# Performance work log

Measured on AMD Instinct MI355X. Metric: run time of the kernel, lower is better.

Reference implementation:

```python
import jax, jax.numpy as jnp
import numpy as np

C = 1.0          # self.c = -curvature = 1.0
SQRT_C = 1.0
EPS = 1e-10
NORM_MAX = 0.99


def setup_inputs() -> dict:
    key = jax.random.key(0)
    k1, k2 = jax.random.split(key)
    b, n, m, d = 4, 4096, 4096, 128
    # scale so points lie inside the Poincare ball (||x|| ~ 0.57 < 1)
    x = jax.random.normal(k1, (b, n, d), dtype=jnp.float32) * 0.05
    y = jax.random.normal(k2, (b, m, d), dtype=jnp.float32) * 0.05
    return {"x": x, "y": y}


def reference(x, y):
    # Pairwise hyperbolic distance d(x_i, y_j) = 2/sqrt(c) * atanh(sqrt(c) * ||(-x_i) (+)_c y_j||)
    # Mobius add: num = A*(-x) + B*y, denom = 1 + 2c<-x,y> + c^2 ||x||^2 ||y||^2
    # with A = 1 + 2c<-x,y> + c||y||^2,  B = 1 - c||x||^2.
    # We never form the (b,n,m,d) tensor: ||A*(-x)+B*y||^2 = A^2||x||^2 - 2AB<x,y> + B^2||y||^2.
    xs = jnp.sum(x * x, axis=-1)                     # (b, n)
    ys = jnp.sum(y * y, axis=-1)                     # (b, m)
    dot = jnp.einsum('bnd,bmd->bnm', x, y)           # (b, n, m) <x_i, y_j>
    xs_ = xs[:, :, None]                             # (b, n, 1)
    ys_ = ys[:, None, :]                             # (b, 1, m)
    A = 1.0 - 2.0 * C * dot + C * ys_                # (b, n, m)
    B = 1.0 - C * xs_                                # (b, n, 1)
    denom = 1.0 - 2.0 * C * dot + (C * C) * xs_ * ys_
    num_sq = A * A * xs_ - 2.0 * A * B * dot + B * B * ys_
    diff_norm = jnp.sqrt(jnp.maximum(num_sq, 0.0)) / jnp.maximum(denom, EPS)
    diff_norm = jnp.clip(diff_norm, EPS, NORM_MAX)
    return (2.0 / SQRT_C) * jnp.arctanh(SQRT_C * diff_norm)
```

## Files before the change

kernel.cpp:

```cpp
#include <hip/hip_runtime.h>
#include <hip/hip_bf16.h>

typedef __bf16 bf16x8 __attribute__((ext_vector_type(8)));
typedef float  f32x4  __attribute__((ext_vector_type(4)));

#define NN 4096
#define DK 128
#define BM 128
#define BN 128
#define NMAX 0.99f
#define LN2F 0.69314718056f

#define WS_XB   0
#define WS_YB   (4u*4096u*DK*2u)
#define WS_XC   (2u*WS_YB)
#define WS_YC   (WS_XC + 4u*4096u*8u)
#define WS_REQ  (WS_YC + 4u*4096u*8u)

__device__ __forceinline__ void load_lds16(const void* g, void* l) {
    __builtin_amdgcn_global_load_lds(
        (const __attribute__((address_space(1))) unsigned int*)g,
        (__attribute__((address_space(3))) unsigned int*)l, 16, 0, 0);
}

__global__ __launch_bounds__(256)
void prep_kernel(const float* __restrict__ X, const float* __restrict__ Y,
                 __bf16* __restrict__ Xb, __bf16* __restrict__ Yb,
                 float2* __restrict__ XC, float2* __restrict__ YC)
{
    const int tid = threadIdx.x;
    const int c16 = tid & 15;
    const int rl  = tid >> 4;
    const int gr  = blockIdx.x * 16 + rl;

    const float* src = blockIdx.y ? Y : X;
    __bf16*      dst = blockIdx.y ? Yb : Xb;
    float2*      nc  = blockIdx.y ? YC : XC;

    const f32x4* s4 = (const f32x4*)(src + (size_t)gr * DK + c16 * 8);
    f32x4 v0 = s4[0], v1 = s4[1];
    float s = v0[0]*v0[0] + v0[1]*v0[1] + v0[2]*v0[2] + v0[3]*v0[3]
            + v1[0]*v1[0] + v1[1]*v1[1] + v1[2]*v1[2] + v1[3]*v1[3];
    s += __shfl_xor(s, 1);
    s += __shfl_xor(s, 2);
    s += __shfl_xor(s, 4);
    s += __shfl_xor(s, 8);

    bf16x8 pk;
    pk[0]=(__bf16)v0[0]; pk[1]=(__bf16)v0[1]; pk[2]=(__bf16)v0[2]; pk[3]=(__bf16)v0[3];
    pk[4]=(__bf16)v1[0]; pk[5]=(__bf16)v1[1]; pk[6]=(__bf16)v1[2]; pk[7]=(__bf16)v1[3];

    const int tile = gr >> 7;
    const int rloc = gr & 127;
    const int byt  = (rloc * 256 + c16 * 16) ^ ((rloc & 7) << 4);
    *(bf16x8*)((char*)(dst + (size_t)tile * (BM * DK)) + byt) = pk;

    if (c16 == 0) nc[gr] = make_float2(s, __logf(1.0f - s));
}

__global__ __launch_bounds__(512, 4)
void hyp_main(const __bf16* __restrict__ Xb, const __bf16* __restrict__ Yb,
              const float2* __restrict__ XC, const float2* __restrict__ YC,
              float* __restrict__ Out)
{
    __shared__ alignas(16) __bf16 aL[BM * DK];
    __shared__ alignas(16) __bf16 bL[BN * DK];
    __shared__ float2 xcL[BM];
    __shared__ float2 ycL[BN];

    const int tid  = threadIdx.x;
    const int lane = tid & 63;
    const int wid  = tid >> 6;
    const int bz   = blockIdx.z;
    const int brow = blockIdx.y * BM;
    const int bcol = blockIdx.x * BN;

    const char* xt = (const char*)(Xb + (size_t)(bz * 32 + blockIdx.y) * (BM * DK));
    const char* yt = (const char*)(Yb + (size_t)(bz * 32 + blockIdx.x) * (BN * DK));

    {
        const int woff = wid * 4096;
#pragma unroll
        for (int j = 0; j < 4; ++j) {
            load_lds16(xt + woff + j * 1024 + lane * 16, (char*)aL + woff + j * 1024);
            load_lds16(yt + woff + j * 1024 + lane * 16, (char*)bL + woff + j * 1024);
        }
    }
    if (tid < 128)       xcL[tid]       = XC[bz * NN + brow + tid];
    else if (tid < 256)  ycL[tid - 128] = YC[bz * NN + bcol + (tid - 128)];
    __syncthreads();

    const int wm  = wid >> 2;
    const int wn  = wid & 3;
    const int r16 = lane & 15;
    const int kg  = lane >> 4;

    f32x4 acc[4][2] = {};

#pragma unroll
    for (int ks = 0; ks < 4; ++ks) {
        const int kb = ks * 32 + kg * 8;
        bf16x8 af[4], bg[2];
#pragma unroll
        for (int i = 0; i < 4; ++i) {
            const int r = wm * 64 + i * 16 + r16;
            const int byt = (r * 256 + kb * 2) ^ ((r & 7) << 4);
            af[i] = *(const bf16x8*)((const char*)aL + byt);
        }
#pragma unroll
        for (int j = 0; j < 2; ++j) {
            const int r = wn * 32 + j * 16 + r16;
            const int byt = (r * 256 + kb * 2) ^ ((r & 7) << 4);
            bg[j] = *(const bf16x8*)((const char*)bL + byt);
        }
#pragma unroll
        for (int i = 0; i < 4; ++i)
#pragma unroll
            for (int j = 0; j < 2; ++j)
                acc[i][j] = __builtin_amdgcn_mfma_f32_16x16x32_bf16(bg[j], af[i], acc[i][j], 0, 0, 0);
    }

    float* ob = Out + ((size_t)bz * NN + brow) * NN + bcol;
#pragma unroll
    for (int i = 0; i < 4; ++i) {
        const int r = wm * 64 + i * 16 + r16;
        const float2 xc = xcL[r];
        const float u = xc.x, cx = xc.y;
        float* orow = ob + (size_t)r * NN;
#pragma unroll
        for (int j = 0; j < 2; ++j) {
            const int cb = wn * 32 + j * 16 + kg * 4;
            const f32x4 y01 = *(const f32x4*)&ycL[cb];
            const f32x4 y23 = *(const f32x4*)&ycL[cb + 2];
            f32x4 o4;
#pragma unroll
            for (int q = 0; q < 4; ++q) {
                const float d  = acc[i][j][q];
                const float v  = (q < 2) ? y01[2 * q] : y23[2 * (q - 2)];
                const float cy = (q < 2) ? y01[2 * q + 1] : y23[2 * (q - 2) + 1];
                const float e1  = fmaf(-2.0f, d, 1.0f);
                const float den = fmaf(u, v, e1);
                float s = fmaf(-2.0f, d, u + v);
                s = fmaxf(s, 1e-12f);
                const float rt  = __builtin_amdgcn_sqrtf(s * den);
                const float arg = fmaf(2.0f, rt, den + s);
                o4[q] = fmaf(__log2f(arg), LN2F, -(cx + cy));
            }
            *(f32x4*)(orow + cb) = o4;
        }
    }
}

__global__ __launch_bounds__(512, 4)
void hyp_fallback(const float* __restrict__ X, const float* __restrict__ Y,
                  float* __restrict__ Out)
{
    __shared__ alignas(16) __bf16 aL[BM * DK];
    __shared__ alignas(16) __bf16 bL[BN * DK];
    __shared__ float xsL[BM];
    __shared__ float ysL[BN];

    const int tid  = threadIdx.x;
    const int bz   = blockIdx.z;
    const int brow = blockIdx.y * BM;
    const int bcol = blockIdx.x * BN;
    const float* xb = X + ((size_t)bz * NN + brow) * DK;
    const float* yb = Y + ((size_t)bz * NN + bcol) * DK;
    const int c16 = tid & 15;
    const int rr  = tid >> 4;

#pragma unroll
    for (int p = 0; p < 4; ++p) {
        const int r = p * 32 + rr;
        const f32x4* s4 = (const f32x4*)(xb + r * DK + c16 * 8);
        f32x4 v0 = s4[0], v1 = s4[1];
        float s = v0[0]*v0[0] + v0[1]*v0[1] + v0[2]*v0[2] + v0[3]*v0[3]
                + v1[0]*v1[0] + v1[1]*v1[1] + v1[2]*v1[2] + v1[3]*v1[3];
        s += __shfl_xor(s, 1); s += __shfl_xor(s, 2);
        s += __shfl_xor(s, 4); s += __shfl_xor(s, 8);
        if (c16 == 0) xsL[r] = s;
        bf16x8 pk;
        pk[0]=(__bf16)v0[0]; pk[1]=(__bf16)v0[1]; pk[2]=(__bf16)v0[2]; pk[3]=(__bf16)v0[3];
        pk[4]=(__bf16)v1[0]; pk[5]=(__bf16)v1[1]; pk[6]=(__bf16)v1[2]; pk[7]=(__bf16)v1[3];
        const int byt = (r * 256 + c16 * 16) ^ ((r & 7) << 4);
        *(bf16x8*)((char*)aL + byt) = pk;
    }
#pragma unroll
    for (int p = 0; p < 4; ++p) {
        const int r = p * 32 + rr;
        const f32x4* s4 = (const f32x4*)(yb + r * DK + c16 * 8);
        f32x4 v0 = s4[0], v1 = s4[1];
        float s = v0[0]*v0[0] + v0[1]*v0[1] + v0[2]*v0[2] + v0[3]*v0[3]
                + v1[0]*v1[0] + v1[1]*v1[1] + v1[2]*v1[2] + v1[3]*v1[3];
        s += __shfl_xor(s, 1); s += __shfl_xor(s, 2);
        s += __shfl_xor(s, 4); s += __shfl_xor(s, 8);
        if (c16 == 0) ysL[r] = s;
        bf16x8 pk;
        pk[0]=(__bf16)v0[0]; pk[1]=(__bf16)v0[1]; pk[2]=(__bf16)v0[2]; pk[3]=(__bf16)v0[3];
        pk[4]=(__bf16)v1[0]; pk[5]=(__bf16)v1[1]; pk[6]=(__bf16)v1[2]; pk[7]=(__bf16)v1[3];
        const int byt = (r * 256 + c16 * 16) ^ ((r & 7) << 4);
        *(bf16x8*)((char*)bL + byt) = pk;
    }
    __syncthreads();

    const int lane = tid & 63;
    const int wid  = tid >> 6;
    const int wm   = wid >> 2;
    const int wn   = wid & 3;
    const int r16  = lane & 15;
    const int kg   = lane >> 4;
    f32x4 acc[4][2] = {};
#pragma unroll
    for (int ks = 0; ks < 4; ++ks) {
        const int kb = ks * 32 + kg * 8;
        bf16x8 af[4], bg[2];
#pragma unroll
        for (int i = 0; i < 4; ++i) {
            const int r = wm * 64 + i * 16 + r16;
            const int byt = (r * 256 + kb * 2) ^ ((r & 7) << 4);
            af[i] = *(const bf16x8*)((const char*)aL + byt);
        }
#pragma unroll
        for (int j = 0; j < 2; ++j) {
            const int r = wn * 32 + j * 16 + r16;
            const int byt = (r * 256 + kb * 2) ^ ((r & 7) << 4);
            bg[j] = *(const bf16x8*)((const char*)bL + byt);
        }
#pragma unroll
        for (int i = 0; i < 4; ++i)
#pragma unroll
            for (int j = 0; j < 2; ++j)
                acc[i][j] = __builtin_amdgcn_mfma_f32_16x16x32_bf16(bg[j], af[i], acc[i][j], 0, 0, 0);
    }
    float* ob = Out + ((size_t)bz * NN + brow) * NN + bcol;
#pragma unroll
    for (int i = 0; i < 4; ++i) {
        const int r = wm * 64 + i * 16 + r16;
        const float u = xsL[r];
        float* orow = ob + (size_t)r * NN;
#pragma unroll
        for (int j = 0; j < 2; ++j) {
            const int cb = wn * 32 + j * 16 + kg * 4;
            const f32x4 v4 = *(const f32x4*)&ysL[cb];
            f32x4 o4;
#pragma unroll
            for (int q = 0; q < 4; ++q) {
                const float d  = acc[i][j][q];
                const float v  = v4[q];
                const float e1 = fmaf(-2.0f, d, 1.0f);
                const float den = fmaf(u, v, e1);
                float s = fmaf(-2.0f, d, u + v);
                s = fmaxf(s, 1e-12f);
                const float dn0 = s * __builtin_amdgcn_rsqf(s * den);
                const float dn = fminf(dn0, NMAX);
                o4[q] = __logf((1.0f + dn) * __builtin_amdgcn_rcpf(1.0f - dn));
            }
            *(f32x4*)(orow + cb) = o4;
        }
    }
}

extern "C" void kernel_launch(void* const* d_in, const int* in_sizes, int n_in,
                              void* d_out, int out_size, void* d_ws, size_t ws_size,
                              hipStream_t stream) {
    const float* X = (const float*)d_in[0];
    const float* Y = (const float*)d_in[1];
    float* O = (float*)d_out;
    const int b = in_sizes[0] / (NN * DK);

    if (ws_size >= WS_REQ) {
        __bf16* Xb = (__bf16*)((char*)d_ws + WS_XB);
        __bf16* Yb = (__bf16*)((char*)d_ws + WS_YB);
        float2* XC = (float2*)((char*)d_ws + WS_XC);
        float2* YC = (float2*)((char*)d_ws + WS_YC);
        dim3 pg(b * NN / 16, 2, 1);
        prep_kernel<<<pg, dim3(256), 0, stream>>>(X, Y, Xb, Yb, XC, YC);
        dim3 grid(NN / BN, NN / BM, b);
        hyp_main<<<grid, dim3(512), 0, stream>>>(Xb, Yb, XC, YC, O);
    } else {
        dim3 grid(NN / BN, NN / BM, b);
        hyp_fallback<<<grid, dim3(512), 0, stream>>>(X, Y, O);
    }
}
```

Baseline: 72.37 us.

## Shrink main kernel tiles to 64x64 with 256 threads and row-streamed MFMA

Cuts the hyp_main output tile from 128x128 to 64x64 and the block from 512 to 256 threads, and updates the prep kernel's tile swizzle to the 64-row layout. B fragments for all k-steps are loaded into registers once, and each 16-row slab is computed and written out in turn, so fewer accumulators are live at a time. The intent is more blocks per CU and better overlap of the store-bound epilogue. The cost is four times as many blocks, each reloading its X and Y tiles, with less reuse per byte loaded. The fallback kernel is pinned to hardcoded 128 sizes.

Result: slower. 78.58 us (+8.6%).

```diff
diff --git a/kernel.cpp b/kernel.cpp
--- a/kernel.cpp
+++ b/kernel.cpp
@@ -6,8 +6,8 @@
 
 #define NN 4096
 #define DK 128
-#define BM 128
-#define BN 128
+#define BM 64
+#define BN 64
 #define NMAX 0.99f
 #define LN2F 0.69314718056f
 
@@ -50,15 +50,15 @@
     pk[0]=(__bf16)v0[0]; pk[1]=(__bf16)v0[1]; pk[2]=(__bf16)v0[2]; pk[3]=(__bf16)v0[3];
     pk[4]=(__bf16)v1[0]; pk[5]=(__bf16)v1[1]; pk[6]=(__bf16)v1[2]; pk[7]=(__bf16)v1[3];
 
-    const int tile = gr >> 7;
-    const int rloc = gr & 127;
+    const int tile = gr >> 6;
+    const int rloc = gr & 63;
     const int byt  = (rloc * 256 + c16 * 16) ^ ((rloc & 7) << 4);
     *(bf16x8*)((char*)(dst + (size_t)tile * (BM * DK)) + byt) = pk;
 
     if (c16 == 0) nc[gr] = make_float2(s, __logf(1.0f - s));
 }
 
-__global__ __launch_bounds__(512, 4)
+__global__ __launch_bounds__(256, 4)
 void hyp_main(const __bf16* __restrict__ Xb, const __bf16* __restrict__ Yb,
               const float2* __restrict__ XC, const float2* __restrict__ YC,
               float* __restrict__ Out)
@@ -75,8 +75,8 @@
     const int brow = blockIdx.y * BM;
     const int bcol = blockIdx.x * BN;
 
-    const char* xt = (const char*)(Xb + (size_t)(bz * 32 + blockIdx.y) * (BM * DK));
-    const char* yt = (const char*)(Yb + (size_t)(bz * 32 + blockIdx.x) * (BN * DK));
+    const char* xt = (const char*)(Xb + (size_t)(bz * 64 + blockIdx.y) * (BM * DK));
+    const char* yt = (const char*)(Yb + (size_t)(bz * 64 + blockIdx.x) * (BN * DK));
 
     {
         const int woff = wid * 4096;
@@ -86,44 +86,44 @@
             load_lds16(yt + woff + j * 1024 + lane * 16, (char*)bL + woff + j * 1024);
         }
     }
-    if (tid < 128)       xcL[tid]       = XC[bz * NN + brow + tid];
-    else if (tid < 256)  ycL[tid - 128] = YC[bz * NN + bcol + (tid - 128)];
+    if (tid < 64)        xcL[tid]      = XC[bz * NN + brow + tid];
+    else if (tid < 128)  ycL[tid - 64] = YC[bz * NN + bcol + (tid - 64)];
     __syncthreads();
 
-    const int wm  = wid >> 2;
-    const int wn  = wid & 3;
+    const int wm  = wid >> 1;
+    const int wn  = wid & 1;
     const int r16 = lane & 15;
     const int kg  = lane >> 4;
 
-    f32x4 acc[4][2] = {};
-
+    bf16x8 bga[4][2];
 #pragma unroll
     for (int ks = 0; ks < 4; ++ks) {
         const int kb = ks * 32 + kg * 8;
-        bf16x8 af[4], bg[2];
-#pragma unroll
-        for (int i = 0; i < 4; ++i) {
-            const int r = wm * 64 + i * 16 + r16;
-            const int byt = (r * 256 + kb * 2) ^ ((r & 7) << 4);
-            af[i] = *(const bf16x8*)((const char*)aL + byt);
-        }
 #pragma unroll
         for (int j = 0; j < 2; ++j) {
             const int r = wn * 32 + j * 16 + r16;
             const int byt = (r * 256 + kb * 2) ^ ((r & 7) << 4);
-            bg[j] = *(const bf16x8*)((const char*)bL + byt);
-        }
-#pragma unroll
-        for (int i = 0; i < 4; ++i)
+            bga[ks][j] = *(const bf16x8*)((const char*)bL + byt);
+        }
+    }
+
+    float* ob = Out + ((size_t)bz * NN + brow) * NN + bcol;
+
+#pragma unroll
+    for (int i = 0; i < 2; ++i) {
+        f32x4 acc[2] = {};
+#pragma unroll
+        for (int ks = 0; ks < 4; ++ks) {
+            const int kb = ks * 32 + kg * 8;
+            const int r  = wm * 32 + i * 16 + r16;
+            const int byt = (r * 256 + kb * 2) ^ ((r & 7) << 4);
+            const bf16x8 af = *(const bf16x8*)((const char*)aL + byt);
 #pragma unroll
             for (int j = 0; j < 2; ++j)
-                acc[i][j] = __builtin_amdgcn_mfma_f32_16x16x32_bf16(bg[j], af[i], acc[i][j], 0, 0, 0);
-    }
-
-    float* ob = Out + ((size_t)bz * NN + brow) * NN + bcol;
-#pragma unroll
-    for (int i = 0; i < 4; ++i) {
-        const int r = wm * 64 + i * 16 + r16;
+                acc[j] = __builtin_amdgcn_mfma_f32_16x16x32_bf16(bga[ks][j], af, acc[j], 0, 0, 0);
+        }
+
+        const int r = wm * 32 + i * 16 + r16;
         const float2 xc = xcL[r];
         const float u = xc.x, cx = xc.y;
         float* orow = ob + (size_t)r * NN;
@@ -135,7 +135,7 @@
             f32x4 o4;
 #pragma unroll
             for (int q = 0; q < 4; ++q) {
-                const float d  = acc[i][j][q];
+                const float d  = acc[j][q];
                 const float v  = (q < 2) ? y01[2 * q] : y23[2 * (q - 2)];
                 const float cy = (q < 2) ? y01[2 * q + 1] : y23[2 * (q - 2) + 1];
                 const float e1  = fmaf(-2.0f, d, 1.0f);
@@ -155,15 +155,15 @@
 void hyp_fallback(const float* __restrict__ X, const float* __restrict__ Y,
                   float* __restrict__ Out)
 {
-    __shared__ alignas(16) __bf16 aL[BM * DK];
-    __shared__ alignas(16) __bf16 bL[BN * DK];
-    __shared__ float xsL[BM];
-    __shared__ float ysL[BN];
+    __shared__ alignas(16) __bf16 aL[128 * DK];
+    __shared__ alignas(16) __bf16 bL[128 * DK];
+    __shared__ float xsL[128];
+    __shared__ float ysL[128];
 
     const int tid  = threadIdx.x;
     const int bz   = blockIdx.z;
-    const int brow = blockIdx.y * BM;
-    const int bcol = blockIdx.x * BN;
+    const int brow = blockIdx.y * 128;
+    const int bcol = blockIdx.x * 128;
     const float* xb = X + ((size_t)bz * NN + brow) * DK;
     const float* yb = Y + ((size_t)bz * NN + bcol) * DK;
     const int c16 = tid & 15;
@@ -276,9 +276,9 @@
         dim3 pg(b * NN / 16, 2, 1);
         prep_kernel<<<pg, dim3(256), 0, stream>>>(X, Y, Xb, Yb, XC, YC);
         dim3 grid(NN / BN, NN / BM, b);
-        hyp_main<<<grid, dim3(512), 0, stream>>>(Xb, Yb, XC, YC, O);
+        hyp_main<<<grid, dim3(256), 0, stream>>>(Xb, Yb, XC, YC, O);
     } else {
-        dim3 grid(NN / BN, NN / BM, b);
+        dim3 grid(NN / 128, NN / 128, b);
         hyp_fallback<<<grid, dim3(512), 0, stream>>>(X, Y, O);
     }
 }
```
